# Kernel optimization log

Measured on AMD Instinct MI355X. Metric: run time of the kernel, lower is better.

The kernel has to match this reference:

```python
import jax, jax.numpy as jnp
import numpy as np

D_MODEL = 1024
N_HEAD = 16
D_FF = 4096
SEG = 128  # hardcoded modality split length in the original module
EPS = 1e-5


def setup_inputs() -> dict:
    key = jax.random.key(0)
    ks = jax.random.split(key, 18)
    s = 0.02
    d, f = D_MODEL, D_FF
    inp = {
        "src": jax.random.normal(ks[0], (128, 256, d), dtype=jnp.float32),
        "Wq": jax.random.normal(ks[1], (d, d), dtype=jnp.float32) * s,
        "bq": jnp.zeros((d,), dtype=jnp.float32),
        "Wk": jax.random.normal(ks[2], (d, d), dtype=jnp.float32) * s,
        "bk": jnp.zeros((d,), dtype=jnp.float32),
        "Wv": jax.random.normal(ks[3], (d, d), dtype=jnp.float32) * s,
        "bv": jnp.zeros((d,), dtype=jnp.float32),
        "Wo": jax.random.normal(ks[4], (d, d), dtype=jnp.float32) * s,
        "bo": jnp.zeros((d,), dtype=jnp.float32),
        "W1": jax.random.normal(ks[5], (d, f), dtype=jnp.float32) * s,
        "b1": jnp.zeros((f,), dtype=jnp.float32),
        "W2": jax.random.normal(ks[6], (f, d), dtype=jnp.float32) * s,
        "b2": jnp.zeros((d,), dtype=jnp.float32),
        "g1": jnp.ones((SEG, d), dtype=jnp.float32),
        "beta1": jnp.zeros((SEG, d), dtype=jnp.float32),
        "g2": jnp.ones((SEG, d), dtype=jnp.float32),
        "beta2": jnp.zeros((SEG, d), dtype=jnp.float32),
    }
    return inp


def _mha(q_in, kv_in, Wq, bq, Wk, bk, Wv, bv, Wo, bo):
    B, Sq, d = q_in.shape
    Sk = kv_in.shape[1]
    dh = d // N_HEAD
    # project and split heads: [B, S, d] -> [B, H, S, dh]
    q = (q_in @ Wq + bq).reshape(B, Sq, N_HEAD, dh).transpose(0, 2, 1, 3)
    k = (kv_in @ Wk + bk).reshape(B, Sk, N_HEAD, dh).transpose(0, 2, 1, 3)
    v = (kv_in @ Wv + bv).reshape(B, Sk, N_HEAD, dh).transpose(0, 2, 1, 3)
    scores = jnp.einsum("bhqd,bhkd->bhqk", q, k) / jnp.sqrt(jnp.float32(dh))
    probs = jax.nn.softmax(scores, axis=-1)
    out = jnp.einsum("bhqk,bhkd->bhqd", probs, v)
    out = out.transpose(0, 2, 1, 3).reshape(B, Sq, d)
    return out @ Wo + bo


def _ln2d(x, g, b):
    # LayerNorm over last two dims (128, d_model), matching nn.LayerNorm((128, d))
    mu = jnp.mean(x, axis=(-2, -1), keepdims=True)
    var = jnp.mean(jnp.square(x - mu), axis=(-2, -1), keepdims=True)
    return (x - mu) * jax.lax.rsqrt(var + EPS) * g + b


def reference(src, Wq, bq, Wk, bk, Wv, bv, Wo, bo, W1, b1, W2, b2, g1, beta1, g2, beta2):
    modal1 = src[:, :SEG, :]
    modal2 = src[:, SEG:, :]

    def ffn(x):
        return jax.nn.relu(x @ W1 + b1) @ W2 + b2

    # modal1 attends to modal2
    m1 = modal1 + _mha(modal1, modal2, Wq, bq, Wk, bk, Wv, bv, Wo, bo)
    m1 = _ln2d(m1, g1, beta1)
    m1 = _ln2d(m1 + ffn(m1), g2, beta2)

    # modal2 attends to updated modal1
    m2 = modal2 + _mha(modal2, m1, Wq, bq, Wk, bk, Wv, bv, Wo, bo)
    m2 = _ln2d(m2, g1, beta1)
    m2 = _ln2d(m2 + ffn(m2), g2, beta2)

    return jnp.concatenate([m1, m2], axis=1)
```

## Files before the change

### kernel.cpp

```cpp
#include <hip/hip_runtime.h>
#include <stdint.h>

#define DEV __device__ __forceinline__

typedef __bf16 bf16x8 __attribute__((ext_vector_type(8)));
typedef float  f32x4  __attribute__((ext_vector_type(4)));

struct alignas(8) U16x4 { uint16_t x, y, z, w; };
struct alignas(16) U16x8 { uint16_t v[8]; };

DEV uint16_t f2bf(float f) {
  union { float f; uint32_t u; } v; v.f = f;
  uint32_t r = v.u + 0x7fffu + ((v.u >> 16) & 1u);
  return (uint16_t)(r >> 16);
}
DEV float bf2f(uint16_t u) {
  union { uint32_t u; float f; } v; v.u = ((uint32_t)u) << 16;
  return v.f;
}

DEV void gload16(const void* g, void* l) {
  __builtin_amdgcn_global_load_lds((__attribute__((address_space(1))) void*)(g),
                                   (__attribute__((address_space(3))) void*)(l),
                                   16, 0, 0);
}

__global__ __launch_bounds__(1024) void transpose_cvt(
    const float* __restrict__ in, uint16_t* __restrict__ out, int R, int C) {
  __shared__ float tile[32][33];
  const int tx = threadIdx.x, ty = threadIdx.y;
  const int r = blockIdx.y * 32 + ty, c = blockIdx.x * 32 + tx;
  tile[ty][tx] = in[(size_t)r * C + c];
  __syncthreads();
  const int oc = blockIdx.x * 32 + ty;
  const int orr = blockIdx.y * 32 + tx;
  out[(size_t)oc * R + orr] = f2bf(tile[tx][ty]);
}

__global__ __launch_bounds__(256) void cvt_modal(
    const float* __restrict__ src, uint16_t* __restrict__ m1, uint16_t* __restrict__ m2) {
  const int idx = blockIdx.x * 256 + threadIdx.x;
  const int E = idx * 4;
  const int t = E >> 10, dd = E & 1023;
  const size_t s1 = ((size_t)(t >> 7) * 256 + (t & 127)) * 1024 + dd;
  float4 a = *(const float4*)&src[s1];
  float4 b = *(const float4*)&src[s1 + 131072];
  U16x4 pa{f2bf(a.x), f2bf(a.y), f2bf(a.z), f2bf(a.w)};
  U16x4 pb{f2bf(b.x), f2bf(b.y), f2bf(b.z), f2bf(b.w)};
  *(U16x4*)&m1[E] = pa;
  *(U16x4*)&m2[E] = pb;
}

#define TILE2(T, ST, WAITSTR)                                                   \
  {                                                                             \
    const int abase = ((T) & 3) * 8192;                                         \
    const int bbase = 32768 + ((T) & 3) * 8192;                                 \
    bf16x8 afr[4], bfr[4];                                                      \
    _Pragma("unroll") for (int n = 0; n < 4; ++n)                               \
        bfr[n] = *(const bf16x8*)&lds[bbase + boff + n * 512];                  \
    _Pragma("unroll") for (int m = 0; m < 4; ++m)                               \
        afr[m] = *(const bf16x8*)&lds[abase + aoff + m * 512];                  \
    asm volatile(WAITSTR ::: "memory");                                         \
    __builtin_amdgcn_s_barrier();                                               \
    if (ST) {                                                                   \
      const int kn = ((T) + 3) << 5;                                            \
      const int sb = (((T) + 3) & 3) * 8192;                                    \
      gload16(gA + kn, &lds[sb + wS]);                                          \
      gload16(gB + kn, &lds[32768 + sb + wS]);                                  \
    }                                                                           \
    asm volatile("s_waitcnt lgkmcnt(0)" ::: "memory");                          \
    __builtin_amdgcn_sched_barrier(0);                                          \
    __builtin_amdgcn_s_setprio(1);                                              \
    _Pragma("unroll") for (int m = 0; m < 4; ++m)                               \
        _Pragma("unroll") for (int n = 0; n < 4; ++n)                           \
        acc[m][n] = __builtin_amdgcn_mfma_f32_16x16x32_bf16(afr[m], bfr[n],     \
                                                            acc[m][n], 0, 0, 0);\
    __builtin_amdgcn_s_setprio(0);                                              \
    __builtin_amdgcn_sched_barrier(0);                                          \
  }

template <int RESID, bool RELU, bool OUTF32>
__global__ __launch_bounds__(1024, 1) void gemm256(
    const uint16_t* __restrict__ A, const uint16_t* __restrict__ Bt,
    const float* __restrict__ bias, const void* __restrict__ resid,
    void* __restrict__ outp, int N, int K, int nbn, int soff) {
  __shared__ __align__(16) uint16_t lds[65536];

  const int nwg = gridDim.x;
  const int s = (blockIdx.x & 7) * (nwg >> 3) + (blockIdx.x >> 3);
  const int bm = s / nbn, bn = s % nbn;
  const int brow = bm << 8, bcol = bn << 8;

  const int tid = threadIdx.x;
  const int w = tid >> 6, lane = tid & 63, l15 = lane & 15, lhi = lane >> 4;
  const int wm = w >> 2, wn = w & 3;

  const int srow = tid >> 2;
  const int cswz = (tid & 3) ^ ((tid >> 3) & 3);
  const uint16_t* gA = A + (size_t)(brow + srow) * K + cswz * 8;
  const uint16_t* gB = Bt + (size_t)(bcol + srow) * K + cswz * 8;
  const int wS = w * 512;

  const int p = lhi ^ ((l15 >> 1) & 3);
  const int aoff = (wm * 64 + l15) * 32 + p * 8;
  const int boff = (wn * 64 + l15) * 32 + p * 8;

  f32x4 acc[4][4];
  const f32x4 z = {0.f, 0.f, 0.f, 0.f};
#pragma unroll
  for (int m = 0; m < 4; ++m)
#pragma unroll
    for (int n = 0; n < 4; ++n) acc[m][n] = z;

  const int nt = K >> 5;

#pragma unroll
  for (int pt = 0; pt < 3; ++pt) {
    const int sb = pt * 8192, kk = pt << 5;
    gload16(gA + kk, &lds[sb + wS]);
    gload16(gB + kk, &lds[32768 + sb + wS]);
  }
  asm volatile("s_waitcnt vmcnt(4)" ::: "memory");
  __builtin_amdgcn_s_barrier();
  __builtin_amdgcn_sched_barrier(0);

  int t = 0;
  for (; t < nt - 3; ++t) TILE2(t, true, "s_waitcnt vmcnt(2)");
  TILE2(t, false, "s_waitcnt vmcnt(2)");
  ++t;
  TILE2(t, false, "s_waitcnt vmcnt(0)");
  ++t;
  TILE2(t, false, "");

#pragma unroll
  for (int n = 0; n < 4; ++n) {
    const int col = bcol + wn * 64 + n * 16 + l15;
    const float bs = bias[col];
#pragma unroll
    for (int m = 0; m < 4; ++m) {
#pragma unroll
      for (int r = 0; r < 4; ++r) {
        const int row = brow + wm * 64 + m * 16 + lhi * 4 + r;
        float v = acc[m][n][r] + bs;
        if (RELU) v = fmaxf(v, 0.f);
        if (RESID == 1) v += ((const float*)resid)[(size_t)row * 1024 + col];
        if (RESID == 2)
          v += ((const float*)resid)[((size_t)(row >> 7) * 256 + soff + (row & 127)) * 1024 + col];
        if (RESID == 3)
          v += bf2f(((const uint16_t*)resid)[(size_t)row * 1024 + col]);
        if (OUTF32)
          ((float*)outp)[(size_t)row * N + col] = v;
        else
          ((uint16_t*)outp)[(size_t)row * N + col] = f2bf(v);
      }
    }
  }
}

__global__ __launch_bounds__(256) void attn_kern(
    const uint16_t* __restrict__ Q, const uint16_t* __restrict__ KV,
    uint16_t* __restrict__ O) {
  __shared__ uint16_t sm[24576];
  uint16_t* sQ = sm;
  uint16_t* sK = sm + 8192;
  uint16_t* sVt = sm + 16384;
  uint16_t* sP = sm;
  const int bh = blockIdx.x, b = bh >> 4, h = bh & 15;
  const int tid = threadIdx.x, w = tid >> 6, lane = tid & 63, l15 = lane & 15, lhi = lane >> 4;
  const size_t base = (size_t)b * 131072 + h * 64;
  const size_t bkv = (size_t)b * 262144 + h * 64;

  for (int i = 0; i < 4; ++i) {
    const int gidx = i * 256 + tid;
    const int row = gidx >> 3, co = (gidx & 7) * 8;
    *(uint4*)&sQ[row * 64 + co] = *(const uint4*)&Q[base + (size_t)row * 1024 + co];
    *(uint4*)&sK[row * 64 + co] = *(const uint4*)&KV[bkv + (size_t)row * 2048 + co];
  }
  {
    const int r = tid >> 1, cb = (tid & 1) * 32;
    for (int jj = 0; jj < 4; ++jj) {
      uint4 vv = *(const uint4*)&KV[bkv + 1024 + (size_t)r * 2048 + cb + jj * 8];
      const uint16_t* e = (const uint16_t*)&vv;
      for (int j = 0; j < 8; ++j) sVt[(cb + jj * 8 + j) * 128 + r] = e[j];
    }
  }
  __syncthreads();

  f32x4 s[2][8];
  const f32x4 z = {0.f, 0.f, 0.f, 0.f};
  for (int m = 0; m < 2; ++m)
    for (int n = 0; n < 8; ++n) s[m][n] = z;
#pragma unroll
  for (int kk = 0; kk < 2; ++kk) {
    bf16x8 aq[2];
#pragma unroll
    for (int m = 0; m < 2; ++m)
      aq[m] = *(const bf16x8*)&sQ[(w * 32 + m * 16 + l15) * 64 + kk * 32 + lhi * 8];
#pragma unroll
    for (int n = 0; n < 8; ++n) {
      bf16x8 bk = *(const bf16x8*)&sK[(n * 16 + l15) * 64 + kk * 32 + lhi * 8];
#pragma unroll
      for (int m = 0; m < 2; ++m)
        s[m][n] = __builtin_amdgcn_mfma_f32_16x16x32_bf16(aq[m], bk, s[m][n], 0, 0, 0);
    }
  }

  for (int m = 0; m < 2; ++m) {
    float mx[4], sum[4];
#pragma unroll
    for (int r = 0; r < 4; ++r) {
      float v = s[m][0][r];
      for (int n = 1; n < 8; ++n) v = fmaxf(v, s[m][n][r]);
      for (int msk = 1; msk < 16; msk <<= 1) v = fmaxf(v, __shfl_xor(v, msk, 64));
      mx[r] = v;
      sum[r] = 0.f;
    }
    for (int n = 0; n < 8; ++n)
      for (int r = 0; r < 4; ++r) {
        float e = __expf((s[m][n][r] - mx[r]) * 0.125f);
        s[m][n][r] = e;
        sum[r] += e;
      }
#pragma unroll
    for (int r = 0; r < 4; ++r) {
      float t = sum[r];
      for (int msk = 1; msk < 16; msk <<= 1) t += __shfl_xor(t, msk, 64);
      sum[r] = 1.f / t;
    }
    for (int n = 0; n < 8; ++n)
      for (int r = 0; r < 4; ++r) s[m][n][r] *= sum[r];
  }
  __syncthreads();

  for (int m = 0; m < 2; ++m)
    for (int n = 0; n < 8; ++n)
      for (int r = 0; r < 4; ++r)
        sP[(w * 32 + m * 16 + lhi * 4 + r) * 128 + n * 16 + l15] = f2bf(s[m][n][r]);
  __syncthreads();

  f32x4 o[2][4];
  for (int m = 0; m < 2; ++m)
    for (int n = 0; n < 4; ++n) o[m][n] = z;
#pragma unroll
  for (int kk = 0; kk < 4; ++kk) {
    bf16x8 ap[2];
#pragma unroll
    for (int m = 0; m < 2; ++m)
      ap[m] = *(const bf16x8*)&sP[(w * 32 + m * 16 + l15) * 128 + kk * 32 + lhi * 8];
#pragma unroll
    for (int n = 0; n < 4; ++n) {
      bf16x8 bv = *(const bf16x8*)&sVt[(n * 16 + l15) * 128 + kk * 32 + lhi * 8];
#pragma unroll
      for (int m = 0; m < 2; ++m)
        o[m][n] = __builtin_amdgcn_mfma_f32_16x16x32_bf16(ap[m], bv, o[m][n], 0, 0, 0);
    }
  }
  for (int m = 0; m < 2; ++m)
    for (int n = 0; n < 4; ++n)
      for (int r = 0; r < 4; ++r) {
        const int q = w * 32 + m * 16 + lhi * 4 + r, c = n * 16 + l15;
        O[base + (size_t)q * 1024 + c] = f2bf(o[m][n][r]);
      }
}

__global__ __launch_bounds__(256) void ln_stats(
    const uint16_t* __restrict__ x, float* __restrict__ pstats) {
  const int b = blockIdx.x >> 2, q = blockIdx.x & 3, tid = threadIdx.x;
  const uint16_t* xb = x + (size_t)b * 131072 + q * 32768;
  float s = 0.f, ss = 0.f;
  for (int i = tid; i < 4096; i += 256) {
    U16x8 v = *(const U16x8*)&xb[i * 8];
#pragma unroll
    for (int j = 0; j < 8; ++j) {
      float f = bf2f(v.v[j]);
      s += f;
      ss += f * f;
    }
  }
#pragma unroll
  for (int m = 1; m < 64; m <<= 1) {
    s += __shfl_xor(s, m, 64);
    ss += __shfl_xor(ss, m, 64);
  }
  __shared__ float red[8];
  const int w = tid >> 6;
  if ((tid & 63) == 0) { red[w] = s; red[4 + w] = ss; }
  __syncthreads();
  if (tid == 0) {
    pstats[blockIdx.x * 2] = red[0] + red[1] + red[2] + red[3];
    pstats[blockIdx.x * 2 + 1] = red[4] + red[5] + red[6] + red[7];
  }
}

template <bool FINAL>
__global__ __launch_bounds__(256) void ln_apply(
    const uint16_t* __restrict__ x, const float* __restrict__ g,
    const float* __restrict__ bet, const float* __restrict__ pstats,
    uint16_t* __restrict__ outbf, float* __restrict__ outf) {
  const int b = blockIdx.x >> 4, c = blockIdx.x & 15, tid = threadIdx.x;
  float S = 0.f, SS = 0.f;
#pragma unroll
  for (int k = 0; k < 4; ++k) {
    S += pstats[b * 8 + k * 2];
    SS += pstats[b * 8 + k * 2 + 1];
  }
  const float mu = S * (1.f / 131072.f);
  const float rs = rsqrtf(SS * (1.f / 131072.f) - mu * mu + 1e-5f);
  const size_t xb = (size_t)b * 131072;
#pragma unroll
  for (int j = 0; j < 4; ++j) {
    const int o = c * 8192 + (j * 256 + tid) * 8;
    U16x8 v = *(const U16x8*)&x[xb + o];
    float4 g0 = *(const float4*)&g[o], g1 = *(const float4*)&g[o + 4];
    float4 b0 = *(const float4*)&bet[o], b1 = *(const float4*)&bet[o + 4];
    float r[8];
    r[0] = (bf2f(v.v[0]) - mu) * rs * g0.x + b0.x;
    r[1] = (bf2f(v.v[1]) - mu) * rs * g0.y + b0.y;
    r[2] = (bf2f(v.v[2]) - mu) * rs * g0.z + b0.z;
    r[3] = (bf2f(v.v[3]) - mu) * rs * g0.w + b0.w;
    r[4] = (bf2f(v.v[4]) - mu) * rs * g1.x + b1.x;
    r[5] = (bf2f(v.v[5]) - mu) * rs * g1.y + b1.y;
    r[6] = (bf2f(v.v[6]) - mu) * rs * g1.z + b1.z;
    r[7] = (bf2f(v.v[7]) - mu) * rs * g1.w + b1.w;
    if (FINAL) {
      float4 o0{r[0], r[1], r[2], r[3]}, o1{r[4], r[5], r[6], r[7]};
      float* of = outf + (size_t)b * 262144 + o;
      *(float4*)&of[0] = o0;
      *(float4*)&of[4] = o1;
      if (outbf) {
        U16x8 u;
#pragma unroll
        for (int i = 0; i < 8; ++i) u.v[i] = f2bf(r[i]);
        *(U16x8*)&outbf[xb + o] = u;
      }
    } else {
      U16x8 u;
#pragma unroll
      for (int i = 0; i < 8; ++i) u.v[i] = f2bf(r[i]);
      *(U16x8*)&outbf[xb + o] = u;
    }
  }
}

extern "C" void kernel_launch(void* const* d_in, const int* in_sizes, int n_in,
                              void* d_out, int out_size, void* d_ws, size_t ws_size,
                              hipStream_t stream) {
  const float* src = (const float*)d_in[0];
  const float* Wq = (const float*)d_in[1];
  const float* bq = (const float*)d_in[2];
  const float* Wk = (const float*)d_in[3];
  const float* bk = (const float*)d_in[4];
  const float* Wv = (const float*)d_in[5];
  const float* bv = (const float*)d_in[6];
  const float* Wo = (const float*)d_in[7];
  const float* bo = (const float*)d_in[8];
  const float* W1 = (const float*)d_in[9];
  const float* b1 = (const float*)d_in[10];
  const float* W2 = (const float*)d_in[11];
  const float* b2 = (const float*)d_in[12];
  const float* g1 = (const float*)d_in[13];
  const float* be1 = (const float*)d_in[14];
  const float* g2 = (const float*)d_in[15];
  const float* be2 = (const float*)d_in[16];
  float* dout = (float*)d_out;
  char* ws = (char*)d_ws;

  const size_t MB = 1024 * 1024;
  uint16_t* wq_t = (uint16_t*)(ws + 0 * MB);
  uint16_t* wkv_t = (uint16_t*)(ws + 2 * MB);
  uint16_t* wv_t = (uint16_t*)(ws + 4 * MB);
  uint16_t* wo_t = (uint16_t*)(ws + 6 * MB);
  uint16_t* w1_t = (uint16_t*)(ws + 8 * MB);
  uint16_t* w2_t = (uint16_t*)(ws + 16 * MB);
  uint16_t* m1bf = (uint16_t*)(ws + 24 * MB);
  uint16_t* mod2 = (uint16_t*)(ws + 56 * MB);
  uint16_t* QB = (uint16_t*)(ws + 88 * MB);
  uint16_t* KVB = (uint16_t*)(ws + 120 * MB);
  uint16_t* ATT = (uint16_t*)(ws + 184 * MB);
  float* bkvp = (float*)(ws + 184 * MB);
  uint16_t* Hbf = QB;
  uint16_t* mod1 = (uint16_t*)(ws + 216 * MB);
  uint16_t* XAb = (uint16_t*)(ws + 248 * MB);
  uint16_t* YBF = (uint16_t*)(ws + 280 * MB);
  float* pstats = (float*)(ws + 312 * MB);

  dim3 tb(32, 32);
  transpose_cvt<<<dim3(32, 32), tb, 0, stream>>>(Wq, wq_t, 1024, 1024);
  transpose_cvt<<<dim3(32, 32), tb, 0, stream>>>(Wk, wkv_t, 1024, 1024);
  transpose_cvt<<<dim3(32, 32), tb, 0, stream>>>(Wv, wv_t, 1024, 1024);
  transpose_cvt<<<dim3(32, 32), tb, 0, stream>>>(Wo, wo_t, 1024, 1024);
  transpose_cvt<<<dim3(128, 32), tb, 0, stream>>>(W1, w1_t, 1024, 4096);
  transpose_cvt<<<dim3(32, 128), tb, 0, stream>>>(W2, w2_t, 4096, 1024);
  cvt_modal<<<16384, 256, 0, stream>>>(src, mod1, mod2);

  auto phase = [&](const uint16_t* qsrc, const uint16_t* kvsrc, int soff,
                   float* out_f, uint16_t* out_bf) {
    gemm256<0, false, false><<<256, 1024, 0, stream>>>(qsrc, wq_t, bq, nullptr, QB,
                                                       1024, 1024, 4, 0);
    hipMemcpyAsync(bkvp, bk, 4096, hipMemcpyDeviceToDevice, stream);
    hipMemcpyAsync(bkvp + 1024, bv, 4096, hipMemcpyDeviceToDevice, stream);
    gemm256<0, false, false><<<512, 1024, 0, stream>>>(kvsrc, wkv_t, bkvp, nullptr, KVB,
                                                       2048, 1024, 8, 0);
    attn_kern<<<2048, 256, 0, stream>>>(QB, KVB, ATT);
    gemm256<2, false, false><<<256, 1024, 0, stream>>>(ATT, wo_t, bo, src, XAb,
                                                       1024, 1024, 4, soff);
    ln_stats<<<512, 256, 0, stream>>>(XAb, pstats);
    ln_apply<false><<<2048, 256, 0, stream>>>(XAb, g1, be1, pstats, YBF, nullptr);
    gemm256<0, true, false><<<1024, 1024, 0, stream>>>(YBF, w1_t, b1, nullptr, Hbf,
                                                       4096, 1024, 16, 0);
    gemm256<3, false, false><<<256, 1024, 0, stream>>>(Hbf, w2_t, b2, YBF, XAb,
                                                       1024, 4096, 4, 0);
    ln_stats<<<512, 256, 0, stream>>>(XAb, pstats);
    ln_apply<true><<<2048, 256, 0, stream>>>(XAb, g2, be2, pstats, out_bf, out_f);
  };

  phase(mod1, mod2, 0, dout, m1bf);
  phase(mod2, m1bf, 128, dout + 131072, nullptr);

  (void)in_sizes; (void)n_in; (void)out_size; (void)ws_size;
}
```

Before: 1.243 ms.

## Restructure GEMM into 8-wave, 8-phase pipeline with K=64 tiles and double buffering

Replaces the 1024-thread 256x256 GEMM with a 512-thread kernel in which each wave computes a 128x64 sub-tile. K tiles grow to 64 with two double-buffered LDS stages, and every iteration is split into eight phases that interleave global-to-LDS loads with MFMA work and use finer waitcnt/barrier points. Launch bounds allow two workgroups per CU, aiming to raise overlap of memory and compute and to improve fragment reuse. It doubles the accumulator registers per thread and makes the schedule more complex, which risks register pressure and races in the buffer reuse.

Result: faster. 1.209 ms (-2.7%).

```diff
diff --git a/kernel.cpp b/kernel.cpp
--- a/kernel.cpp
+++ b/kernel.cpp
@@ -51,36 +51,59 @@
   *(U16x4*)&m2[E] = pb;
 }
 
-#define TILE2(T, ST, WAITSTR)                                                   \
-  {                                                                             \
-    const int abase = ((T) & 3) * 8192;                                         \
-    const int bbase = 32768 + ((T) & 3) * 8192;                                 \
-    bf16x8 afr[4], bfr[4];                                                      \
-    _Pragma("unroll") for (int n = 0; n < 4; ++n)                               \
-        bfr[n] = *(const bf16x8*)&lds[bbase + boff + n * 512];                  \
-    _Pragma("unroll") for (int m = 0; m < 4; ++m)                               \
-        afr[m] = *(const bf16x8*)&lds[abase + aoff + m * 512];                  \
-    asm volatile(WAITSTR ::: "memory");                                         \
-    __builtin_amdgcn_s_barrier();                                               \
-    if (ST) {                                                                   \
-      const int kn = ((T) + 3) << 5;                                            \
-      const int sb = (((T) + 3) & 3) * 8192;                                    \
-      gload16(gA + kn, &lds[sb + wS]);                                          \
-      gload16(gB + kn, &lds[32768 + sb + wS]);                                  \
-    }                                                                           \
-    asm volatile("s_waitcnt lgkmcnt(0)" ::: "memory");                          \
-    __builtin_amdgcn_sched_barrier(0);                                          \
-    __builtin_amdgcn_s_setprio(1);                                              \
-    _Pragma("unroll") for (int m = 0; m < 4; ++m)                               \
-        _Pragma("unroll") for (int n = 0; n < 4; ++n)                           \
-        acc[m][n] = __builtin_amdgcn_mfma_f32_16x16x32_bf16(afr[m], bfr[n],     \
-                                                            acc[m][n], 0, 0, 0);\
-    __builtin_amdgcn_s_setprio(0);                                              \
-    __builtin_amdgcn_sched_barrier(0);                                          \
+#define STA8(D, H, C, T) \
+  gload16(gA + ((H) * 2 + (C)) * kr64 + (size_t)(T) * 64, \
+          &lds[(D) * 16384 + (H) * 8192 + (C) * 4096 + wS])
+#define STB8(D, H, C, T) \
+  gload16(gB + ((H) * 2 + (C)) * kr64 + (size_t)(T) * 64, \
+          &lds[32768 + (D) * 16384 + (H) * 8192 + (C) * 4096 + wS])
+
+#define PH8(Q, AB, BB, RDB, S1, S2, VMSTR)                                     \
+  {                                                                            \
+    if (RDB) {                                                                 \
+      _Pragma("unroll") for (int n = 0; n < 4; ++n) {                          \
+        bfr[n][0] = *(const bf16x8*)&lds[(BB) + bRow + n * 1024 + c0];         \
+        bfr[n][1] = *(const bf16x8*)&lds[(BB) + bRow + n * 1024 + c1];         \
+      }                                                                        \
+    }                                                                          \
+    _Pragma("unroll") for (int dm = 0; dm < 2; ++dm) {                         \
+      afr[dm][0] = *(const bf16x8*)&lds[(AB) + aRow + ((Q) * 2 + dm) * 1024 + c0]; \
+      afr[dm][1] = *(const bf16x8*)&lds[(AB) + aRow + ((Q) * 2 + dm) * 1024 + c1]; \
+    }                                                                          \
+    S1;                                                                        \
+    S2;                                                                        \
+    __builtin_amdgcn_s_barrier();                                              \
+    asm volatile("s_waitcnt lgkmcnt(0)" ::: "memory");                         \
+    __builtin_amdgcn_sched_barrier(0);                                         \
+    __builtin_amdgcn_s_setprio(1);                                             \
+    _Pragma("unroll") for (int dm = 0; dm < 2; ++dm)                           \
+      _Pragma("unroll") for (int n = 0; n < 4; ++n) {                          \
+        acc[(Q) * 2 + dm][n] = __builtin_amdgcn_mfma_f32_16x16x32_bf16(        \
+            afr[dm][0], bfr[n][0], acc[(Q) * 2 + dm][n], 0, 0, 0);             \
+        acc[(Q) * 2 + dm][n] = __builtin_amdgcn_mfma_f32_16x16x32_bf16(        \
+            afr[dm][1], bfr[n][1], acc[(Q) * 2 + dm][n], 0, 0, 0);             \
+      }                                                                        \
+    __builtin_amdgcn_s_setprio(0);                                             \
+    __builtin_amdgcn_sched_barrier(0);                                         \
+    asm volatile(VMSTR ::: "memory");                                          \
+    __builtin_amdgcn_s_barrier();                                              \
+  }
+
+#define ITER8(I, ST, VM4, VM8)                                                 \
+  {                                                                            \
+    const int t1 = 2 * (I) + 1, t2 = 2 * (I) + 2, t3 = 2 * (I) + 3;            \
+    PH8(0, 0, 32768, 1, STA8(1, 0, 0, t1), STA8(1, 0, 1, t1), "")              \
+    PH8(1, 0, 32768, 0, STA8(1, 1, 0, t1), STA8(1, 1, 1, t1), "")              \
+    PH8(2, 0, 32768, 0, if (ST) STB8(0, 0, 0, t2), if (ST) STB8(0, 0, 1, t2), "") \
+    PH8(3, 0, 32768, 0, if (ST) STB8(0, 1, 0, t2), if (ST) STB8(0, 1, 1, t2), VM4) \
+    PH8(0, 16384, 49152, 1, if (ST) STA8(0, 0, 0, t2), if (ST) STA8(0, 0, 1, t2), "") \
+    PH8(1, 16384, 49152, 0, if (ST) STA8(0, 1, 0, t2), if (ST) STA8(0, 1, 1, t2), "") \
+    PH8(2, 16384, 49152, 0, if (ST) STB8(1, 0, 0, t3), if (ST) STB8(1, 0, 1, t3), "") \
+    PH8(3, 16384, 49152, 0, if (ST) STB8(1, 1, 0, t3), if (ST) STB8(1, 1, 1, t3), VM8) \
   }
 
 template <int RESID, bool RELU, bool OUTF32>
-__global__ __launch_bounds__(1024, 1) void gemm256(
+__global__ __launch_bounds__(512, 2) void gemm8p(
     const uint16_t* __restrict__ A, const uint16_t* __restrict__ Bt,
     const float* __restrict__ bias, const void* __restrict__ resid,
     void* __restrict__ outp, int N, int K, int nbn, int soff) {
@@ -95,52 +118,51 @@
   const int w = tid >> 6, lane = tid & 63, l15 = lane & 15, lhi = lane >> 4;
   const int wm = w >> 2, wn = w & 3;
 
-  const int srow = tid >> 2;
-  const int cswz = (tid & 3) ^ ((tid >> 3) & 3);
-  const uint16_t* gA = A + (size_t)(brow + srow) * K + cswz * 8;
-  const uint16_t* gB = Bt + (size_t)(bcol + srow) * K + cswz * 8;
+  const int cswz = (tid & 7) ^ ((tid >> 3) & 7);
+  const size_t Kz = (size_t)K;
+  const size_t kr64 = 64 * Kz;
+  const uint16_t* gA = A + (size_t)(brow + (tid >> 3)) * Kz + cswz * 8;
+  const uint16_t* gB = Bt + (size_t)(bcol + (tid >> 3)) * Kz + cswz * 8;
   const int wS = w * 512;
 
-  const int p = lhi ^ ((l15 >> 1) & 3);
-  const int aoff = (wm * 64 + l15) * 32 + p * 8;
-  const int boff = (wn * 64 + l15) * 32 + p * 8;
-
-  f32x4 acc[4][4];
+  const int c0 = (lhi ^ (l15 & 7)) * 8;
+  const int c1 = c0 ^ 32;
+  const int aRow = (wm * 128 + l15) * 64;
+  const int bRow = (wn * 64 + l15) * 64;
+
+  f32x4 acc[8][4];
   const f32x4 z = {0.f, 0.f, 0.f, 0.f};
 #pragma unroll
-  for (int m = 0; m < 4; ++m)
+  for (int m = 0; m < 8; ++m)
 #pragma unroll
     for (int n = 0; n < 4; ++n) acc[m][n] = z;
 
-  const int nt = K >> 5;
-
-#pragma unroll
-  for (int pt = 0; pt < 3; ++pt) {
-    const int sb = pt * 8192, kk = pt << 5;
-    gload16(gA + kk, &lds[sb + wS]);
-    gload16(gB + kk, &lds[32768 + sb + wS]);
-  }
+  const int NI = K >> 7;
+
+  STA8(0, 0, 0, 0); STA8(0, 0, 1, 0); STA8(0, 1, 0, 0); STA8(0, 1, 1, 0);
+  STB8(0, 0, 0, 0); STB8(0, 0, 1, 0); STB8(0, 1, 0, 0); STB8(0, 1, 1, 0);
+  STB8(1, 0, 0, 1); STB8(1, 0, 1, 1); STB8(1, 1, 0, 1); STB8(1, 1, 1, 1);
   asm volatile("s_waitcnt vmcnt(4)" ::: "memory");
   __builtin_amdgcn_s_barrier();
   __builtin_amdgcn_sched_barrier(0);
 
-  int t = 0;
-  for (; t < nt - 3; ++t) TILE2(t, true, "s_waitcnt vmcnt(2)");
-  TILE2(t, false, "s_waitcnt vmcnt(2)");
-  ++t;
-  TILE2(t, false, "s_waitcnt vmcnt(0)");
-  ++t;
-  TILE2(t, false, "");
+  {
+    bf16x8 afr[2][2], bfr[4][2];
+    int i = 0;
+    for (; i < NI - 1; ++i)
+      ITER8(i, true, "s_waitcnt vmcnt(4)", "s_waitcnt vmcnt(4)")
+    ITER8(i, false, "s_waitcnt vmcnt(0)", "")
+  }
 
 #pragma unroll
   for (int n = 0; n < 4; ++n) {
     const int col = bcol + wn * 64 + n * 16 + l15;
     const float bs = bias[col];
 #pragma unroll
-    for (int m = 0; m < 4; ++m) {
+    for (int m = 0; m < 8; ++m) {
 #pragma unroll
       for (int r = 0; r < 4; ++r) {
-        const int row = brow + wm * 64 + m * 16 + lhi * 4 + r;
+        const int row = brow + wm * 128 + m * 16 + lhi * 4 + r;
         float v = acc[m][n][r] + bs;
         if (RELU) v = fmaxf(v, 0.f);
         if (RESID == 1) v += ((const float*)resid)[(size_t)row * 1024 + col];
@@ -395,21 +417,21 @@
 
   auto phase = [&](const uint16_t* qsrc, const uint16_t* kvsrc, int soff,
                    float* out_f, uint16_t* out_bf) {
-    gemm256<0, false, false><<<256, 1024, 0, stream>>>(qsrc, wq_t, bq, nullptr, QB,
-                                                       1024, 1024, 4, 0);
+    gemm8p<0, false, false><<<256, 512, 0, stream>>>(qsrc, wq_t, bq, nullptr, QB,
+                                                     1024, 1024, 4, 0);
     hipMemcpyAsync(bkvp, bk, 4096, hipMemcpyDeviceToDevice, stream);
     hipMemcpyAsync(bkvp + 1024, bv, 4096, hipMemcpyDeviceToDevice, stream);
-    gemm256<0, false, false><<<512, 1024, 0, stream>>>(kvsrc, wkv_t, bkvp, nullptr, KVB,
-                                                       2048, 1024, 8, 0);
+    gemm8p<0, false, false><<<512, 512, 0, stream>>>(kvsrc, wkv_t, bkvp, nullptr, KVB,
+                                                     2048, 1024, 8, 0);
     attn_kern<<<2048, 256, 0, stream>>>(QB, KVB, ATT);
-    gemm256<2, false, false><<<256, 1024, 0, stream>>>(ATT, wo_t, bo, src, XAb,
-                                                       1024, 1024, 4, soff);
+    gemm8p<2, false, false><<<256, 512, 0, stream>>>(ATT, wo_t, bo, src, XAb,
+                                                     1024, 1024, 4, soff);
     ln_stats<<<512, 256, 0, stream>>>(XAb, pstats);
     ln_apply<false><<<2048, 256, 0, stream>>>(XAb, g1, be1, pstats, YBF, nullptr);
-    gemm256<0, true, false><<<1024, 1024, 0, stream>>>(YBF, w1_t, b1, nullptr, Hbf,
-                                                       4096, 1024, 16, 0);
-    gemm256<3, false, false><<<256, 1024, 0, stream>>>(Hbf, w2_t, b2, YBF, XAb,
-                                                       1024, 4096, 4, 0);
+    gemm8p<0, true, false><<<1024, 512, 0, stream>>>(YBF, w1_t, b1, nullptr, Hbf,
+                                                     4096, 1024, 16, 0);
+    gemm8p<3, false, false><<<256, 512, 0, stream>>>(Hbf, w2_t, b2, YBF, XAb,
+                                                     1024, 4096, 4, 0);
     ln_stats<<<512, 256, 0, stream>>>(XAb, pstats);
     ln_apply<true><<<2048, 256, 0, stream>>>(XAb, g2, be2, pstats, out_bf, out_f);
   };
```
